# Performance work log

Hardware: AMD Instinct MI355X
Metric: run time of the kernel (lower is better)

## Reference

```python
import jax, jax.numpy as jnp
import numpy as np

B, N, C = 4, 2048, 768
H = 12
D = C // H  # head_dim = 64
SCALE = D ** -0.5


def setup_inputs() -> dict:
    key = jax.random.key(0)
    ks = jax.random.split(key, 9)
    x_q = jax.random.normal(ks[0], (B, N, C), dtype=jnp.float32)
    x_k = jax.random.normal(ks[1], (B, N, C), dtype=jnp.float32)
    x_v = jax.random.normal(ks[2], (B, N, C), dtype=jnp.float32)
    x_u = jax.random.uniform(ks[3], (B, N, C), dtype=jnp.float32)
    s = C ** -0.5
    Wq = jax.random.normal(ks[4], (C, C), dtype=jnp.float32) * s
    Wk = jax.random.normal(ks[5], (C, C), dtype=jnp.float32) * s
    Wv = jax.random.normal(ks[6], (C, C), dtype=jnp.float32) * s
    Wp = jax.random.normal(ks[7], (C, C), dtype=jnp.float32) * s
    bp = jax.random.normal(ks[8], (C,), dtype=jnp.float32) * 0.01
    return {"x_q": x_q, "x_k": x_k, "x_v": x_v, "x_u": x_u,
            "Wq": Wq, "Wk": Wk, "Wv": Wv, "Wp": Wp, "bp": bp}


def reference(x_q, x_k, x_v, x_u, Wq, Wk, Wv, Wp, bp):
    # Linear projections (torch Linear: y = x @ W.T), split into heads [B,H,N,D]
    def to_heads(x, W):
        y = jnp.einsum('bnc,oc->bno', x, W)
        return y.reshape(B, N, H, D).transpose(0, 2, 1, 3)
    q = to_heads(x_q, Wq) * SCALE
    k = to_heads(x_k, Wk)
    v = to_heads(x_v, Wv)
    # Scores [B,H,N,N]
    attn = jnp.einsum('bhqd,bhkd->bhqk', q, k)
    # Uncertainty map: per-query scalar (mean over channels), broadcast over keys & heads
    uc = jnp.mean(x_u, axis=-1)  # [B,N]
    attn = attn * uc[:, None, :, None]
    attn = jax.nn.softmax(attn, axis=-1)
    out = jnp.einsum('bhqk,bhkd->bhqd', attn, v)
    out = out.transpose(0, 2, 1, 3).reshape(B, N, C)
    return jnp.einsum('bnc,oc->bno', out, Wp) + bp
```

## Files before the change

### kernel.cpp

```cpp
#include <hip/hip_runtime.h>
#include <hip/hip_bf16.h>
#include <cstdint>

#define B_ 4
#define N_ 2048
#define C_ 768
#define H_ 12
#define D_ 64
#define QSCALE 0.18033688011112042f

typedef __bf16 bf16x8 __attribute__((ext_vector_type(8)));
typedef float f32x4 __attribute__((ext_vector_type(4)));
typedef float f32x16 __attribute__((ext_vector_type(16)));

__device__ __forceinline__ unsigned f2bs(float x) {
  unsigned u = __builtin_bit_cast(unsigned, x);
  unsigned r = (u + 0x7fffu + ((u >> 16) & 1u)) >> 16;
  return r;
}

__device__ __forceinline__ bf16x8 ldb8(const unsigned short* p) {
  return __builtin_bit_cast(bf16x8, *(const uint4*)p);
}

__device__ __forceinline__ f32x4 mfma16(bf16x8 a, bf16x8 b, f32x4 c) {
  return __builtin_amdgcn_mfma_f32_16x16x32_bf16(a, b, c, 0, 0, 0);
}

__device__ __forceinline__ f32x16 mfma32(bf16x8 a, bf16x8 b, f32x16 c) {
  return __builtin_amdgcn_mfma_f32_32x32x16_bf16(a, b, c, 0, 0, 0);
}

__device__ __forceinline__ void async16(const unsigned short* g, unsigned short* l) {
  __builtin_amdgcn_global_load_lds(
      (const __attribute__((address_space(1))) unsigned int*)g,
      (__attribute__((address_space(3))) unsigned int*)l, 16, 0, 0);
}

__global__ void prep_kernel(
    const float* __restrict__ xq, const float* __restrict__ xk,
    const float* __restrict__ xv, const float* __restrict__ xu,
    const float* __restrict__ Wq, const float* __restrict__ Wk,
    const float* __restrict__ Wv, const float* __restrict__ Wp,
    unsigned short* __restrict__ dxq, unsigned short* __restrict__ dxk,
    unsigned short* __restrict__ dxv,
    unsigned short* __restrict__ dwq, unsigned short* __restrict__ dwk,
    unsigned short* __restrict__ dwv, unsigned short* __restrict__ dwp,
    float* __restrict__ uc) {
  const int id = blockIdx.x;
  if (id < 18432) {
    const float* s = (id < 6144) ? xq : (id < 12288) ? xk : xv;
    unsigned short* d = (id < 6144) ? dxq : (id < 12288) ? dxk : dxv;
    int i = ((id % 6144) * 256 + threadIdx.x) * 4;
    float4 v = *(const float4*)(s + i);
    ushort4 h;
    h.x = (unsigned short)f2bs(v.x); h.y = (unsigned short)f2bs(v.y);
    h.z = (unsigned short)f2bs(v.z); h.w = (unsigned short)f2bs(v.w);
    *(ushort4*)(d + i) = h;
  } else if (id < 20736) {
    int sub = id - 18432;
    int which = sub / 576;
    const float* s = (which == 0) ? Wq : (which == 1) ? Wk : (which == 2) ? Wv : Wp;
    unsigned short* d = (which == 0) ? dwq : (which == 1) ? dwk : (which == 2) ? dwv : dwp;
    int i = ((sub % 576) * 256 + threadIdx.x) * 4;
    float4 v = *(const float4*)(s + i);
    ushort4 h;
    h.x = (unsigned short)f2bs(v.x); h.y = (unsigned short)f2bs(v.y);
    h.z = (unsigned short)f2bs(v.z); h.w = (unsigned short)f2bs(v.w);
    *(ushort4*)(d + i) = h;
  } else {
    int sub = id - 20736;
    int w = threadIdx.x >> 6, lane = threadIdx.x & 63;
    int row = sub * 4 + w;
    const float* p = xu + (size_t)row * C_;
    float s = 0.f;
#pragma unroll
    for (int i = 0; i < 3; ++i) {
      float4 v = *(const float4*)(p + (i * 64 + lane) * 4);
      s += v.x + v.y + v.z + v.w;
    }
#pragma unroll
    for (int off = 1; off < 64; off <<= 1) s += __shfl_xor(s, off);
    if (lane == 0) uc[row] = s * (1.f / 768.f);
  }
}

__device__ __forceinline__ void gemm_mainloop(
    const unsigned short* __restrict__ A, const unsigned short* __restrict__ W,
    int m0, int n0, unsigned short* Al, unsigned short* Bl,
    int tid, int wm, int wn, int quad, int id15, f32x4 (*acc)[4]) {
  const int wb = tid & 192;
  const unsigned short* ap[4];
  const unsigned short* bp[4];
#pragma unroll
  for (int s = 0; s < 4; ++s) {
    int g = s * 256 + tid;
    int row = (g >> 2) & 127;
    int col = ((g >> 9) << 5) | ((g & 3) << 3);
    ap[s] = A + (size_t)(m0 + row) * C_ + col;
    bp[s] = W + (size_t)(n0 + row) * C_ + col;
  }

  for (int kt = 0; kt < C_; kt += 64) {
    __syncthreads();
#pragma unroll
    for (int s = 0; s < 4; ++s) {
      async16(ap[s] + kt, Al + (s * 256 + wb) * 8);
      async16(bp[s] + kt, Bl + (s * 256 + wb) * 8);
    }
    __syncthreads();

#pragma unroll
    for (int kk = 0; kk < 2; ++kk) {
      bf16x8 af[4], bfr[4];
#pragma unroll
      for (int i = 0; i < 4; ++i)
        af[i]  = ldb8(&Al[kk * 4096 + (wm + i * 16 + id15) * 32 + quad * 8]);
#pragma unroll
      for (int j = 0; j < 4; ++j)
        bfr[j] = ldb8(&Bl[kk * 4096 + (wn + j * 16 + id15) * 32 + quad * 8]);
#pragma unroll
      for (int i = 0; i < 4; ++i)
#pragma unroll
        for (int j = 0; j < 4; ++j)
          acc[i][j] = mfma16(af[i], bfr[j], acc[i][j]);
    }
  }
}

#define TSTR 136
__global__ __launch_bounds__(256, 3) void gemm_qkv(
    const unsigned short* __restrict__ xq, const unsigned short* __restrict__ xk,
    const unsigned short* __restrict__ xv,
    const unsigned short* __restrict__ wq, const unsigned short* __restrict__ wk,
    const unsigned short* __restrict__ wv,
    unsigned short* __restrict__ oq, unsigned short* __restrict__ ok,
    unsigned short* __restrict__ ov, const float* __restrict__ uc) {
  __shared__ __align__(16) unsigned short S[128 * TSTR];
  unsigned short* Al = S;
  unsigned short* Bl = S + 8192;
  const int tid = threadIdx.x;
  const int w = tid >> 6, lane = tid & 63, quad = lane >> 4, id15 = lane & 15;
  const int wm = (w >> 1) << 6, wn = (w & 1) << 6;
  const int id = blockIdx.x;
  const int xcd = id & 7, slot = id >> 3;
  const int n0 = (slot % 6) << 7;
  const int gz = xcd * 24 + slot / 6;
  const int z = gz >> 6, m0 = (gz & 63) << 7;

  const unsigned short* A = (z == 0) ? xq : (z == 1) ? xk : xv;
  const unsigned short* W = (z == 0) ? wq : (z == 1) ? wk : wv;

  f32x4 acc[4][4] = {};
  gemm_mainloop(A, W, m0, n0, Al, Bl, tid, wm, wn, quad, id15, acc);

  if (z == 2) {
    __syncthreads();
#pragma unroll
    for (int i = 0; i < 4; ++i)
#pragma unroll
      for (int j = 0; j < 4; ++j) {
        uint2 u;
        u.x = f2bs(acc[i][j][0]) | (f2bs(acc[i][j][1]) << 16);
        u.y = f2bs(acc[i][j][2]) | (f2bs(acc[i][j][3]) << 16);
        *(uint2*)&S[(wn + j * 16 + id15) * TSTR + wm + i * 16 + quad * 4] = u;
      }
    __syncthreads();
    const int b = m0 >> 11, nb = m0 & (N_ - 1);
#pragma unroll
    for (int s = 0; s < 8; ++s) {
      int c = s * 256 + tid;
      int row = c >> 4, o = (c & 15) << 3;
      *(uint4*)(ov + (size_t)(b * C_ + n0 + row) * N_ + nb + o) = *(const uint4*)&S[row * TSTR + o];
    }
    return;
  }

#pragma unroll
  for (int i = 0; i < 4; ++i) {
#pragma unroll
    for (int j = 0; j < 4; ++j) {
#pragma unroll
      for (int r = 0; r < 4; ++r) {
        int gm = m0 + wm + i * 16 + quad * 4 + r;
        int gn = n0 + wn + j * 16 + id15;
        float v = acc[i][j][r];
        if (z == 0) {
          v *= QSCALE * uc[gm];
          oq[(size_t)gm * C_ + gn] = (unsigned short)f2bs(v);
        } else {
          ok[(size_t)gm * C_ + gn] = (unsigned short)f2bs(v);
        }
      }
    }
  }
}

__global__ __launch_bounds__(256, 4) void gemm_out(
    const unsigned short* __restrict__ ao, const unsigned short* __restrict__ wp,
    float* __restrict__ out, const float* __restrict__ bias) {
  __shared__ __align__(16) unsigned short Al[64 * 64];
  __shared__ __align__(16) unsigned short Bl[128 * 64];
  const int tid = threadIdx.x;
  const int w = tid >> 6, lane = tid & 63, quad = lane >> 4, id15 = lane & 15;
  const int wm = (w >> 1) << 5, wn = (w & 1) << 6;
  const int id = blockIdx.x;
  const int xcd = id & 7, slot = id >> 3;
  const int n0 = (slot % 6) << 7;
  const int m0 = (xcd * 16 + slot / 6) << 6;

  const int wb = tid & 192;
  const unsigned short* ap[2];
#pragma unroll
  for (int s = 0; s < 2; ++s) {
    int g = s * 256 + tid;
    int row = (g >> 2) & 63;
    int col = ((g >> 8) << 5) | ((g & 3) << 3);
    ap[s] = ao + (size_t)(m0 + row) * C_ + col;
  }
  const unsigned short* bp[4];
#pragma unroll
  for (int s = 0; s < 4; ++s) {
    int g = s * 256 + tid;
    int row = (g >> 2) & 127;
    int col = ((g >> 9) << 5) | ((g & 3) << 3);
    bp[s] = wp + (size_t)(n0 + row) * C_ + col;
  }

  f32x4 acc[2][4] = {};
  for (int kt = 0; kt < C_; kt += 64) {
    __syncthreads();
#pragma unroll
    for (int s = 0; s < 2; ++s) async16(ap[s] + kt, Al + (s * 256 + wb) * 8);
#pragma unroll
    for (int s = 0; s < 4; ++s) async16(bp[s] + kt, Bl + (s * 256 + wb) * 8);
    __syncthreads();

#pragma unroll
    for (int kk = 0; kk < 2; ++kk) {
      bf16x8 af[2], bfr[4];
#pragma unroll
      for (int i = 0; i < 2; ++i)
        af[i]  = ldb8(&Al[kk * 2048 + (wm + i * 16 + id15) * 32 + quad * 8]);
#pragma unroll
      for (int j = 0; j < 4; ++j)
        bfr[j] = ldb8(&Bl[kk * 4096 + (wn + j * 16 + id15) * 32 + quad * 8]);
#pragma unroll
      for (int i = 0; i < 2; ++i)
#pragma unroll
        for (int j = 0; j < 4; ++j)
          acc[i][j] = mfma16(af[i], bfr[j], acc[i][j]);
    }
  }

#pragma unroll
  for (int i = 0; i < 2; ++i) {
#pragma unroll
    for (int j = 0; j < 4; ++j) {
#pragma unroll
      for (int r = 0; r < 4; ++r) {
        int gm = m0 + wm + i * 16 + quad * 4 + r;
        int gn = n0 + wn + j * 16 + id15;
        out[(size_t)gm * C_ + gn] = acc[i][j][r] + bias[gn];
      }
    }
  }
}

#define KSTR 72
#define VOFF (64 * KSTR)
#define BUFO (2 * 64 * KSTR)
__global__ __launch_bounds__(256, 3) void attn_kernel(
    const unsigned short* __restrict__ Q, const unsigned short* __restrict__ Kk,
    const unsigned short* __restrict__ Vt, unsigned short* __restrict__ O) {
  __shared__ __align__(16) unsigned short KV[2 * 2 * 64 * KSTR];

  const int tid = threadIdx.x;
  const int w = tid >> 6, lane = tid & 63;
  const int i32 = lane & 31, hi = lane >> 5;
  const int id = blockIdx.x;
  const int xcd = id & 7, slot = id >> 3;
  const int bh = xcd * 6 + (slot >> 4);
  const int qt = slot & 15;
  const int b = bh / H_, h = bh % H_;
  const int q0 = qt * 128 + w * 32;

  bf16x8 qf[4];
#pragma unroll
  for (int s = 0; s < 4; ++s)
    qf[s] = ldb8(Q + (size_t)(b * N_ + q0 + i32) * C_ + h * 64 + s * 16 + hi * 8);

  const uint4 onesu = {0x3F803F80u, 0x3F803F80u, 0x3F803F80u, 0x3F803F80u};
  const bf16x8 onesf = __builtin_bit_cast(bf16x8, onesu);

  f32x16 oacc0 = {}, oacc1 = {}, lacc = {};

  const size_t kbase = (size_t)(b * N_) * C_ + h * 64;
  const size_t vbase = (size_t)(b * C_ + h * 64) * N_;
  const int srow0 = tid >> 3, srow1 = 32 + (tid >> 3);
  const int sseg = (tid & 7) << 3;

  {
    uint4 a0 = *(const uint4*)(Kk + kbase + (size_t)srow0 * C_ + sseg);
    uint4 a1 = *(const uint4*)(Kk + kbase + (size_t)srow1 * C_ + sseg);
    uint4 c0 = *(const uint4*)(Vt + vbase + (size_t)srow0 * N_ + sseg);
    uint4 c1 = *(const uint4*)(Vt + vbase + (size_t)srow1 * N_ + sseg);
    *(uint4*)&KV[srow0 * KSTR + sseg] = a0;
    *(uint4*)&KV[srow1 * KSTR + sseg] = a1;
    *(uint4*)&KV[VOFF + srow0 * KSTR + sseg] = c0;
    *(uint4*)&KV[VOFF + srow1 * KSTR + sseg] = c1;
  }

  int cur = 0;
  for (int kc = 0; kc < N_; kc += 64) {
    const bool last = (kc + 64 >= N_);
    uint4 a0, a1, c0, c1;
    if (!last) {
      const int kcn = kc + 64;
      a0 = *(const uint4*)(Kk + kbase + (size_t)(kcn + srow0) * C_ + sseg);
      a1 = *(const uint4*)(Kk + kbase + (size_t)(kcn + srow1) * C_ + sseg);
      c0 = *(const uint4*)(Vt + vbase + (size_t)srow0 * N_ + kcn + sseg);
      c1 = *(const uint4*)(Vt + vbase + (size_t)srow1 * N_ + kcn + sseg);
    }

    asm volatile("s_waitcnt lgkmcnt(0)" ::: "memory");
    __builtin_amdgcn_s_barrier();

    const unsigned short* Kc = KV + (cur ? BUFO : 0);
    const unsigned short* Vc = Kc + VOFF;

    f32x16 sA = {}, sB = {};
    __builtin_amdgcn_s_setprio(1);
#pragma unroll
    for (int s = 0; s < 4; ++s) {
      bf16x8 kf = ldb8(Kc + i32 * KSTR + s * 16 + hi * 8);
      sA = mfma32(kf, qf[s], sA);
    }
#pragma unroll
    for (int s = 0; s < 4; ++s) {
      bf16x8 kf = ldb8(Kc + (32 + i32) * KSTR + s * 16 + hi * 8);
      sB = mfma32(kf, qf[s], sB);
    }
    __builtin_amdgcn_s_setprio(0);

#pragma unroll
    for (int t = 0; t < 2; ++t) {
      f32x16 s16 = (t == 0) ? sA : sB;
      bf16x8 vf0[2], vf1[2];
#pragma unroll
      for (int sl = 0; sl < 2; ++sl) {
        vf0[sl] = ldb8(Vc + i32 * KSTR + (2 * t + sl) * 16 + hi * 8);
        vf1[sl] = ldb8(Vc + (32 + i32) * KSTR + (2 * t + sl) * 16 + hi * 8);
      }
      unsigned Dw[8];
#pragma unroll
      for (int j = 0; j < 8; ++j) {
        float e0 = exp2f(s16[2 * j]);
        float e1 = exp2f(s16[2 * j + 1]);
        unsigned d;
        asm("v_cvt_pk_bf16_f32 %0, %1, %2" : "=v"(d) : "v"(e0), "v"(e1));
        Dw[j] = d;
      }
      __builtin_amdgcn_s_setprio(1);
#pragma unroll
      for (int sl = 0; sl < 2; ++sl) {
        const int bb = sl * 4;
        unsigned x0 = Dw[bb + 0], y0 = Dw[bb + 2];
        unsigned x1 = Dw[bb + 1], y1 = Dw[bb + 3];
        asm("v_permlane32_swap_b32 %0, %1" : "+v"(x0), "+v"(y0));
        asm("v_permlane32_swap_b32 %0, %1" : "+v"(x1), "+v"(y1));
        uint4 u;
        u.x = x0;
        u.y = x1;
        u.z = y0;
        u.w = y1;
        bf16x8 pf = __builtin_bit_cast(bf16x8, u);
        lacc = mfma32(pf, onesf, lacc);
        oacc0 = mfma32(pf, vf0[sl], oacc0);
        oacc1 = mfma32(pf, vf1[sl], oacc1);
      }
      __builtin_amdgcn_s_setprio(0);
    }

    if (!last) {
      unsigned short* Kn = KV + (cur ? 0 : BUFO);
      *(uint4*)&Kn[srow0 * KSTR + sseg] = a0;
      *(uint4*)&Kn[srow1 * KSTR + sseg] = a1;
      *(uint4*)&Kn[VOFF + srow0 * KSTR + sseg] = c0;
      *(uint4*)&Kn[VOFF + srow1 * KSTR + sseg] = c1;
    }
    cur ^= 1;
  }

#pragma unroll
  for (int r = 0; r < 16; ++r) {
    float linv = 1.0f / lacc[r];
    int q = q0 + (r & 3) + 8 * (r >> 2) + 4 * hi;
    size_t base = (size_t)(b * N_ + q) * C_ + h * 64 + i32;
    O[base] = (unsigned short)f2bs(oacc0[r] * linv);
    O[base + 32] = (unsigned short)f2bs(oacc1[r] * linv);
  }
}

extern "C" void kernel_launch(void* const* d_in, const int* in_sizes, int n_in,
                              void* d_out, int out_size, void* d_ws, size_t ws_size,
                              hipStream_t stream) {
  const float* x_q = (const float*)d_in[0];
  const float* x_k = (const float*)d_in[1];
  const float* x_v = (const float*)d_in[2];
  const float* x_u = (const float*)d_in[3];
  const float* Wq  = (const float*)d_in[4];
  const float* Wk  = (const float*)d_in[5];
  const float* Wv  = (const float*)d_in[6];
  const float* Wp  = (const float*)d_in[7];
  const float* bp  = (const float*)d_in[8];

  char* ws = (char*)d_ws;
  size_t off = 0;
  auto alloc = [&](size_t bytes) {
    char* p = ws + off;
    off += (bytes + 255) & ~(size_t)255;
    return p;
  };
  unsigned short* wq16 = (unsigned short*)alloc((size_t)C_ * C_ * 2);
  unsigned short* wk16 = (unsigned short*)alloc((size_t)C_ * C_ * 2);
  unsigned short* wv16 = (unsigned short*)alloc((size_t)C_ * C_ * 2);
  unsigned short* wp16 = (unsigned short*)alloc((size_t)C_ * C_ * 2);
  float*          ucp  = (float*)alloc((size_t)B_ * N_ * 4);
  unsigned short* xq16 = (unsigned short*)alloc((size_t)B_ * N_ * C_ * 2);
  unsigned short* xk16 = (unsigned short*)alloc((size_t)B_ * N_ * C_ * 2);
  unsigned short* xv16 = (unsigned short*)alloc((size_t)B_ * N_ * C_ * 2);
  unsigned short* q_s  = (unsigned short*)alloc((size_t)B_ * N_ * C_ * 2);
  unsigned short* k_s  = (unsigned short*)alloc((size_t)B_ * N_ * C_ * 2);
  unsigned short* vT   = (unsigned short*)alloc((size_t)B_ * N_ * C_ * 2);
  unsigned short* ao   = (unsigned short*)alloc((size_t)B_ * N_ * C_ * 2);

  prep_kernel<<<dim3(22784), 256, 0, stream>>>(x_q, x_k, x_v, x_u, Wq, Wk, Wv, Wp,
                                               xq16, xk16, xv16,
                                               wq16, wk16, wv16, wp16, ucp);
  gemm_qkv<<<dim3(1152), 256, 0, stream>>>(xq16, xk16, xv16, wq16, wk16, wv16,
                                           q_s, k_s, vT, ucp);
  attn_kernel<<<dim3(768), 256, 0, stream>>>(q_s, k_s, vT, ao);
  gemm_out<<<dim3(768), 256, 0, stream>>>(ao, wp16, (float*)d_out, bp);
}
```

Before: 300.7 us.

## Split attention warps over query and key halves to reuse K fragments

```diff
diff --git a/kernel.cpp b/kernel.cpp
--- a/kernel.cpp
+++ b/kernel.cpp
@@ -270,7 +270,7 @@
 #define KSTR 72
 #define VOFF (64 * KSTR)
 #define BUFO (2 * 64 * KSTR)
-__global__ __launch_bounds__(256, 3) void attn_kernel(
+__global__ __launch_bounds__(256, 2) void attn_kernel(
     const unsigned short* __restrict__ Q, const unsigned short* __restrict__ Kk,
     const unsigned short* __restrict__ Vt, unsigned short* __restrict__ O) {
   __shared__ __align__(16) unsigned short KV[2 * 2 * 64 * KSTR];
@@ -278,27 +278,32 @@
   const int tid = threadIdx.x;
   const int w = tid >> 6, lane = tid & 63;
   const int i32 = lane & 31, hi = lane >> 5;
+  const int wq = w & 1, wk = w >> 1;
   const int id = blockIdx.x;
   const int xcd = id & 7, slot = id >> 3;
   const int bh = xcd * 6 + (slot >> 4);
   const int qt = slot & 15;
   const int b = bh / H_, h = bh % H_;
-  const int q0 = qt * 128 + w * 32;
-
-  bf16x8 qf[4];
-#pragma unroll
-  for (int s = 0; s < 4; ++s)
-    qf[s] = ldb8(Q + (size_t)(b * N_ + q0 + i32) * C_ + h * 64 + s * 16 + hi * 8);
+  const int q0 = qt * 128 + wq * 64;
+
+  bf16x8 qfA[4], qfB[4];
+#pragma unroll
+  for (int s = 0; s < 4; ++s) {
+    qfA[s] = ldb8(Q + (size_t)(b * N_ + q0 + i32) * C_ + h * 64 + s * 16 + hi * 8);
+    qfB[s] = ldb8(Q + (size_t)(b * N_ + q0 + 32 + i32) * C_ + h * 64 + s * 16 + hi * 8);
+  }
 
   const uint4 onesu = {0x3F803F80u, 0x3F803F80u, 0x3F803F80u, 0x3F803F80u};
   const bf16x8 onesf = __builtin_bit_cast(bf16x8, onesu);
 
-  f32x16 oacc0 = {}, oacc1 = {}, lacc = {};
+  f32x16 o0A = {}, o1A = {}, lA = {};
+  f32x16 o0B = {}, o1B = {}, lB = {};
 
   const size_t kbase = (size_t)(b * N_) * C_ + h * 64;
   const size_t vbase = (size_t)(b * C_ + h * 64) * N_;
   const int srow0 = tid >> 3, srow1 = 32 + (tid >> 3);
   const int sseg = (tid & 7) << 3;
+  const int krow = wk * 32 + i32;
 
   {
     uint4 a0 = *(const uint4*)(Kk + kbase + (size_t)srow0 * C_ + sseg);
@@ -310,6 +315,35 @@
     *(uint4*)&KV[VOFF + srow0 * KSTR + sseg] = c0;
     *(uint4*)&KV[VOFF + srow1 * KSTR + sseg] = c1;
   }
+
+  auto softmax_pv = [&](const f32x16& s16, bf16x8 vf0[2], bf16x8 vf1[2],
+                        f32x16& lac, f32x16& oa0, f32x16& oa1) {
+    unsigned Dw[8];
+#pragma unroll
+    for (int j = 0; j < 8; ++j) {
+      float e0 = exp2f(s16[2 * j]);
+      float e1 = exp2f(s16[2 * j + 1]);
+      unsigned d;
+      asm("v_cvt_pk_bf16_f32 %0, %1, %2" : "=v"(d) : "v"(e0), "v"(e1));
+      Dw[j] = d;
+    }
+    __builtin_amdgcn_s_setprio(1);
+#pragma unroll
+    for (int sl = 0; sl < 2; ++sl) {
+      const int bb = sl * 4;
+      unsigned x0 = Dw[bb + 0], y0 = Dw[bb + 2];
+      unsigned x1 = Dw[bb + 1], y1 = Dw[bb + 3];
+      asm("v_permlane32_swap_b32 %0, %1" : "+v"(x0), "+v"(y0));
+      asm("v_permlane32_swap_b32 %0, %1" : "+v"(x1), "+v"(y1));
+      uint4 u;
+      u.x = x0; u.y = x1; u.z = y0; u.w = y1;
+      bf16x8 pf = __builtin_bit_cast(bf16x8, u);
+      lac = mfma32(pf, onesf, lac);
+      oa0 = mfma32(pf, vf0[sl], oa0);
+      oa1 = mfma32(pf, vf1[sl], oa1);
+    }
+    __builtin_amdgcn_s_setprio(0);
+  };
 
   int cur = 0;
   for (int kc = 0; kc < N_; kc += 64) {
@@ -329,58 +363,27 @@
     const unsigned short* Kc = KV + (cur ? BUFO : 0);
     const unsigned short* Vc = Kc + VOFF;
 
+    bf16x8 kf[4];
     f32x16 sA = {}, sB = {};
     __builtin_amdgcn_s_setprio(1);
 #pragma unroll
-    for (int s = 0; s < 4; ++s) {
-      bf16x8 kf = ldb8(Kc + i32 * KSTR + s * 16 + hi * 8);
-      sA = mfma32(kf, qf[s], sA);
-    }
-#pragma unroll
-    for (int s = 0; s < 4; ++s) {
-      bf16x8 kf = ldb8(Kc + (32 + i32) * KSTR + s * 16 + hi * 8);
-      sB = mfma32(kf, qf[s], sB);
-    }
+    for (int s = 0; s < 4; ++s)
+      kf[s] = ldb8(Kc + krow * KSTR + s * 16 + hi * 8);
+#pragma unroll
+    for (int s = 0; s < 4; ++s) sA = mfma32(kf[s], qfA[s], sA);
+#pragma unroll
+    for (int s = 0; s < 4; ++s) sB = mfma32(kf[s], qfB[s], sB);
     __builtin_amdgcn_s_setprio(0);
 
-#pragma unroll
-    for (int t = 0; t < 2; ++t) {
-      f32x16 s16 = (t == 0) ? sA : sB;
-      bf16x8 vf0[2], vf1[2];
-#pragma unroll
-      for (int sl = 0; sl < 2; ++sl) {
-        vf0[sl] = ldb8(Vc + i32 * KSTR + (2 * t + sl) * 16 + hi * 8);
-        vf1[sl] = ldb8(Vc + (32 + i32) * KSTR + (2 * t + sl) * 16 + hi * 8);
-      }
-      unsigned Dw[8];
-#pragma unroll
-      for (int j = 0; j < 8; ++j) {
-        float e0 = exp2f(s16[2 * j]);
-        float e1 = exp2f(s16[2 * j + 1]);
-        unsigned d;
-        asm("v_cvt_pk_bf16_f32 %0, %1, %2" : "=v"(d) : "v"(e0), "v"(e1));
-        Dw[j] = d;
-      }
-      __builtin_amdgcn_s_setprio(1);
-#pragma unroll
-      for (int sl = 0; sl < 2; ++sl) {
-        const int bb = sl * 4;
-        unsigned x0 = Dw[bb + 0], y0 = Dw[bb + 2];
-        unsigned x1 = Dw[bb + 1], y1 = Dw[bb + 3];
-        asm("v_permlane32_swap_b32 %0, %1" : "+v"(x0), "+v"(y0));
-        asm("v_permlane32_swap_b32 %0, %1" : "+v"(x1), "+v"(y1));
-        uint4 u;
-        u.x = x0;
-        u.y = x1;
-        u.z = y0;
-        u.w = y1;
-        bf16x8 pf = __builtin_bit_cast(bf16x8, u);
-        lacc = mfma32(pf, onesf, lacc);
-        oacc0 = mfma32(pf, vf0[sl], oacc0);
-        oacc1 = mfma32(pf, vf1[sl], oacc1);
-      }
-      __builtin_amdgcn_s_setprio(0);
-    }
+    bf16x8 vf0[2], vf1[2];
+#pragma unroll
+    for (int sl = 0; sl < 2; ++sl) {
+      vf0[sl] = ldb8(Vc + i32 * KSTR + (2 * wk + sl) * 16 + hi * 8);
+      vf1[sl] = ldb8(Vc + (32 + i32) * KSTR + (2 * wk + sl) * 16 + hi * 8);
+    }
+
+    softmax_pv(sA, vf0, vf1, lA, o0A, o1A);
+    softmax_pv(sB, vf0, vf1, lB, o0B, o1B);
 
     if (!last) {
       unsigned short* Kn = KV + (cur ? 0 : BUFO);
@@ -392,14 +395,38 @@
     cur ^= 1;
   }
 
-#pragma unroll
-  for (int r = 0; r < 16; ++r) {
-    float linv = 1.0f / lacc[r];
-    int q = q0 + (r & 3) + 8 * (r >> 2) + 4 * hi;
-    size_t base = (size_t)(b * N_ + q) * C_ + h * 64 + i32;
-    O[base] = (unsigned short)f2bs(oacc0[r] * linv);
-    O[base + 32] = (unsigned short)f2bs(oacc1[r] * linv);
-  }
+  float* Pf = (float*)KV;
+  const int pbase = (wq * 64 + lane) * 48;
+
+  auto combine = [&](const f32x16& oa0, const f32x16& oa1, const f32x16& lac,
+                     int qoff) {
+    __syncthreads();
+    if (wk == 1) {
+#pragma unroll
+      for (int r = 0; r < 16; ++r) {
+        Pf[pbase + r] = oa0[r];
+        Pf[pbase + 16 + r] = oa1[r];
+        Pf[pbase + 32 + r] = lac[r];
+      }
+    }
+    __syncthreads();
+    if (wk == 0) {
+#pragma unroll
+      for (int r = 0; r < 16; ++r) {
+        float v0 = oa0[r] + Pf[pbase + r];
+        float v1 = oa1[r] + Pf[pbase + 16 + r];
+        float lv = lac[r] + Pf[pbase + 32 + r];
+        float linv = 1.0f / lv;
+        int q = q0 + qoff + (r & 3) + 8 * (r >> 2) + 4 * hi;
+        size_t base = (size_t)(b * N_ + q) * C_ + h * 64 + i32;
+        O[base] = (unsigned short)f2bs(v0 * linv);
+        O[base + 32] = (unsigned short)f2bs(v1 * linv);
+      }
+    }
+  };
+
+  combine(o0A, o1A, lA, 0);
+  combine(o0B, o1B, lB, 32);
 }
 
 extern "C" void kernel_launch(void* const* d_in, const int* in_sizes, int n_in,
```

Result: no change. 305.6 us (+1.6%).
